# Kernel optimization log

Hardware: AMD Instinct MI355X
Metric: run time of the kernel (lower is better)

## Reference

```python
import jax, jax.numpy as jnp
import numpy as np

P, M, N, D, H, DFF = 20000, 20000, 16, 128, 8, 512
DPH = D // H
EPS = 1e-6
LN_EPS = 1e-5


def vn_linear(x, w):
    # x: (..., C_in, 3), w: (C_in, C_out) -> (..., C_out, 3)
    return jnp.einsum('...ci,co->...oi', x, w)


def vn_layernorm(x, gamma, beta):
    # x: (P, D, 3); layernorm over channel dim on vector norms, rescale directions
    n = jnp.linalg.norm(x, axis=-1)                      # (P, D)
    mu = jnp.mean(n, axis=-1, keepdims=True)
    var = jnp.var(n, axis=-1, keepdims=True)
    n_hat = (n - mu) / jnp.sqrt(var + LN_EPS) * gamma + beta
    return x * (n_hat / (n + EPS))[..., None]


def vn_relu(q, k):
    # VN nonlinearity: q, k: (..., C, 3); project q off negative half-space of k
    dot = jnp.sum(q * k, axis=-1, keepdims=True)         # (..., C, 1)
    ksq = jnp.sum(k * k, axis=-1, keepdims=True)
    return jnp.where(dot >= 0, q, q - (dot / (ksq + EPS)) * k)


def setup_inputs():
    key = jax.random.key(0)
    ks = jax.random.split(key, 24)
    s = lambda i, shp, scale: (jax.random.normal(ks[i], shp, jnp.float32) * scale)
    inp = {
        'tgt': s(0, (P, D * 3), 1.0),
        'memory': s(1, (M, D * 3), 1.0),
        'sh': s(2, (P, N + 1, 3), 1.0),
        'dist_atten': s(3, (P, N, H), 1.0),
        'Wq': s(4, (D, D), D ** -0.5),
        'Wk': s(5, (D, D), D ** -0.5),
        'Wv': s(6, (D, D), D ** -0.5),
        'Wo': s(7, (D, D), D ** -0.5),
        'g_w1': s(8, (D, H), D ** -0.5),
        'g_b1': jnp.zeros((H,), jnp.float32),
        'g_w2': s(9, (H, H), H ** -0.5),
        'g_b2': jnp.zeros((H,), jnp.float32),
        'ln1_g': jnp.ones((D,), jnp.float32),
        'ln1_b': jnp.zeros((D,), jnp.float32),
        'ln2_g': jnp.ones((D,), jnp.float32),
        'ln2_b': jnp.zeros((D,), jnp.float32),
        'ff_w1': s(10, (D, DFF), D ** -0.5),
        'ff_d1': s(11, (D, DFF), D ** -0.5),
        'ff_w2': s(12, (DFF, D), DFF ** -0.5),
        'index_pair': jax.random.randint(ks[13], (P, N), 0, M),
        'cnt1': jax.random.randint(ks[14], (P,), 0, N),
        'cnt2': jax.random.randint(ks[15], (P,), 0, N),
    }
    return inp


def reference(tgt, memory, sh, dist_atten, Wq, Wk, Wv, Wo,
              g_w1, g_b1, g_w2, g_b2, ln1_g, ln1_b, ln2_g, ln2_b,
              ff_w1, ff_d1, ff_w2, index_pair, cnt1, cnt2):
    x = tgt.reshape(P, D, 3)
    mem = memory.reshape(M, D, 3)
    q = vn_linear(x, Wq)                                  # (P, D, 3)
    k_all = vn_linear(mem, Wk)                            # (M, D, 3)
    v_all = vn_linear(mem, Wv)
    # irregular neighbor gather (ca_attention_mapper_v3)
    k = k_all[index_pair]                                 # (P, N, D, 3)
    v = v_all[index_pair]                                 # (P, N, D, 3)
    sh_n = sh[:, 1:].reshape(P, N, 1, 3)                  # drop l=0 term
    # multi-head dot attention on 3D vector features
    dot_atten = jnp.einsum('phdi,pnhdi->pnh',
                           q.reshape(P, H, DPH, 3),
                           k.reshape(P, N, H, DPH, 3))
    # spherical-harmonic position bias
    pos = jnp.sum((k - q[:, None]) * sh_n, axis=-1)       # (P, N, D)
    pos = jax.nn.relu(pos @ g_w1 + g_b1) @ g_w2 + g_b2    # (P, N, H)
    atten = (dot_atten + pos + dist_atten) / (DPH ** 0.5)
    atten = jax.nn.softmax(atten, axis=1)                 # softmax over neighbors
    tgt2 = jnp.einsum('pnh,pnhci->phci', atten,
                      v.reshape(P, N, H, DPH, 3)).reshape(P, D, 3)
    tgt2 = vn_linear(tgt2, Wo)
    y = vn_layernorm(x + tgt2, ln1_g, ln1_b)
    h1 = vn_relu(vn_linear(y, ff_w1), vn_linear(y, ff_d1))
    ff_out = vn_linear(h1, ff_w2)
    y = vn_layernorm(y + ff_out, ln2_g, ln2_b)
    return y.reshape(P, D * 3)
```

## Files before the change

### kernel.cpp

```cpp
#include <hip/hip_runtime.h>

#define PP 20000

typedef short short8 __attribute__((ext_vector_type(8)));
typedef float floatx4 __attribute__((ext_vector_type(4)));

__device__ __forceinline__ unsigned int bf16_rne_bits(float x){
    unsigned int xb = __float_as_uint(x);
    return (xb + 0x7FFFu + ((xb >> 16) & 1u)) & 0xFFFF0000u;
}
__device__ __forceinline__ void split2(float x, short &h, short &l){
    unsigned int hb = bf16_rne_bits(x);
    h = (short)(hb >> 16);
    float r = x - __uint_as_float(hb);
    l = (short)(bf16_rne_bits(r) >> 16);
}

__device__ __align__(16) short g_ff1[32*8192];
__device__ __align__(16) short g_ff2[16*8192];
__device__ __align__(16) short g_qkvo[4][4*8192];
__device__ __align__(16) float g_vvf[PP*128*4];

__global__ __launch_bounds__(256) void prep_weights(
    const float* __restrict__ Wq, const float* __restrict__ Wk,
    const float* __restrict__ Wv, const float* __restrict__ Wo,
    const float* __restrict__ W1, const float* __restrict__ Wd,
    const float* __restrict__ W2)
{
    const int tid = blockIdx.x*256 + threadIdx.x;
    for (int e = tid; e < 65536; e += 16384){
        int j = e & 7, kg = (e>>3) & 15, n = (e>>7) & 15, ch = e >> 11;
        int k = kg*8 + j, col = ch*16 + n;
        int pos = n*128 + ((kg ^ (n&7)) << 3) + j;
        short h, l;
        split2(W1[(size_t)k*512 + col], h, l);
        g_ff1[ch*8192 + pos]        = h;
        g_ff1[ch*8192 + 2048 + pos] = l;
        split2(Wd[(size_t)k*512 + col], h, l);
        g_ff1[ch*8192 + 4096 + pos] = h;
        g_ff1[ch*8192 + 6144 + pos] = l;
    }
    for (int e = tid; e < 65536; e += 16384){
        int w = e & 31, n2 = (e>>5) & 127, pair = e >> 12;
        int lslot = (w>>3) ^ ((n2>>1)&3);
        int k = pair*32 + lslot*8 + (w&7);
        short h, l; split2(W2[(size_t)k*128 + n2], h, l);
        g_ff2[pair*8192 + n2*32 + w]        = h;
        g_ff2[pair*8192 + 4096 + n2*32 + w] = l;
    }
    for (int e = tid; e < 65536; e += 16384){
        int w = e & 127, col = (e>>7) & 31, ch = (e>>12) & 3, wg = e >> 14;
        int lslot = (w>>3) ^ (col&7);
        int k = lslot*8 + (w&7);
        const float* Wsrc = (wg==0)?Wq:(wg==1)?Wk:(wg==2)?Wv:Wo;
        short h, l; split2(Wsrc[(size_t)k*128 + ch*32 + col], h, l);
        g_qkvo[wg][ch*8192 + col*128 + w]        = h;
        g_qkvo[wg][ch*8192 + 4096 + col*128 + w] = l;
    }
}

template<int VOUT>
__global__ __launch_bounds__(256) void vn_gemm_mfma_t(const float* __restrict__ in,
    int widx, float* __restrict__ out)
{
    __shared__ __align__(16) char pool[32768];
    short* Ysh = (short*)pool;
    short* Ysl = (short*)(pool + 16384);
    short* Bh  = (short*)pool;
    short* Bl  = (short*)(pool + 8192);

    const int tid  = threadIdx.x;
    const int wv   = tid >> 6;
    const int lane = tid & 63;
    const int mrow = lane & 15;
    const int kgrp = lane >> 4;
    const int p0   = blockIdx.x * 16;

    for (int f = tid; f < 2048; f += 256){
        int row = (f >> 7)*4 + 3, k = f & 127;
        Ysh[row*128 + k] = 0; Ysl[row*128 + k] = 0;
    }
    #pragma unroll
    for (int t = 0; t < 6; ++t){
        int f = tid + t*256;
        float4 w4 = *(const float4*)(in + (size_t)p0*384 + f*4);
        int e = f*4, pl = e/384, rem = e - pl*384;
        float vv4[4] = {w4.x, w4.y, w4.z, w4.w};
        #pragma unroll
        for (int j=0;j<4;++j){
            int c = (rem+j)/3, i = (rem+j) - c*3;
            int row = pl*4 + i;
            int idx = row*128 + (((c>>3) ^ (row&7)) << 3) + (c&7);
            short h, l; split2(vv4[j], h, l);
            Ysh[idx] = h; Ysl[idx] = l;
        }
    }
    __syncthreads();
    short8 ahf[4], alf[4];
    {
        const int arow = wv*16 + mrow;
        #pragma unroll
        for (int ks=0;ks<4;++ks){
            int slot = ks*4 + kgrp;
            int aoff = arow*128 + ((slot ^ (arow&7)) << 3);
            ahf[ks] = *(const short8*)(Ysh + aoff);
            alf[ks] = *(const short8*)(Ysl + aoff);
        }
    }

    const short* gW = g_qkvo[widx];
    for (int ch = 0; ch < 4; ++ch){
        __syncthreads();
        #pragma unroll
        for (int t=0;t<4;++t)
            ((short8*)pool)[tid + t*256] =
                ((const short8*)(gW + ch*8192))[tid + t*256];
        __syncthreads();

        #pragma unroll
        for (int ntl=0; ntl<2; ++ntl){
            floatx4 acc = {0.f,0.f,0.f,0.f};
            const int lcol = ntl*16 + mrow;
            #pragma unroll
            for (int ks=0;ks<4;++ks){
                int slot = ks*4 + kgrp;
                int boff = lcol*128 + ((slot ^ (mrow&7)) << 3);
                short8 bh = *(const short8*)(Bh + boff);
                short8 bl = *(const short8*)(Bl + boff);
                acc = __builtin_amdgcn_mfma_f32_16x16x32_bf16(ahf[ks], bh, acc, 0,0,0);
                acc = __builtin_amdgcn_mfma_f32_16x16x32_bf16(ahf[ks], bl, acc, 0,0,0);
                acc = __builtin_amdgcn_mfma_f32_16x16x32_bf16(alf[ks], bh, acc, 0,0,0);
            }
            const int p = p0 + wv*4 + kgrp;
            const int o = ch*32 + ntl*16 + mrow;
            if (VOUT == 0){
                size_t base = (size_t)p*384 + (size_t)o*3;
                out[base    ] = acc[0];
                out[base + 1] = acc[1];
                out[base + 2] = acc[2];
            } else {
                float4 v4;
                v4.x = acc[0]; v4.y = acc[1]; v4.z = acc[2]; v4.w = 0.f;
                *(float4*)(g_vvf + ((size_t)p*128 + o)*4) = v4;
            }
        }
    }
}

__global__ __launch_bounds__(256) void vn_gemm_ln_mfma(const float* __restrict__ in,
    const float* __restrict__ resid, const float* __restrict__ gamma,
    const float* __restrict__ beta, float* __restrict__ out)
{
    __shared__ __align__(16) char pool[32768];
    short* Ysh = (short*)pool;
    short* Ysl = (short*)(pool + 16384);
    short* Bh  = (short*)pool;
    short* Bl  = (short*)(pool + 8192);

    const int tid  = threadIdx.x;
    const int wv   = tid >> 6;
    const int lane = tid & 63;
    const int mrow = lane & 15;
    const int kgrp = lane >> 4;
    const int p0   = blockIdx.x * 16;

    for (int f = tid; f < 2048; f += 256){
        int row = (f >> 7)*4 + 3, k = f & 127;
        Ysh[row*128 + k] = 0; Ysl[row*128 + k] = 0;
    }
    #pragma unroll
    for (int t = 0; t < 6; ++t){
        int f = tid + t*256;
        float4 w4 = *(const float4*)(in + (size_t)p0*384 + f*4);
        int e = f*4, pl = e/384, rem = e - pl*384;
        float vv4[4] = {w4.x, w4.y, w4.z, w4.w};
        #pragma unroll
        for (int j=0;j<4;++j){
            int c = (rem+j)/3, i = (rem+j) - c*3;
            int row = pl*4 + i;
            int idx = row*128 + (((c>>3) ^ (row&7)) << 3) + (c&7);
            short h, l; split2(vv4[j], h, l);
            Ysh[idx] = h; Ysl[idx] = l;
        }
    }
    __syncthreads();
    short8 ahf[4], alf[4];
    {
        const int arow = wv*16 + mrow;
        #pragma unroll
        for (int ks=0;ks<4;++ks){
            int slot = ks*4 + kgrp;
            int aoff = arow*128 + ((slot ^ (arow&7)) << 3);
            ahf[ks] = *(const short8*)(Ysh + aoff);
            alf[ks] = *(const short8*)(Ysl + aoff);
        }
    }

    const int p = p0 + wv*4 + kgrp;
    float rx[8], ry[8], rz[8];
    const short* gW = g_qkvo[3];
    #pragma unroll
    for (int ch = 0; ch < 4; ++ch){
        __syncthreads();
        #pragma unroll
        for (int t=0;t<4;++t)
            ((short8*)pool)[tid + t*256] =
                ((const short8*)(gW + ch*8192))[tid + t*256];
        __syncthreads();

        #pragma unroll
        for (int ntl=0; ntl<2; ++ntl){
            floatx4 acc = {0.f,0.f,0.f,0.f};
            const int lcol = ntl*16 + mrow;
            #pragma unroll
            for (int ks=0;ks<4;++ks){
                int slot = ks*4 + kgrp;
                int boff = lcol*128 + ((slot ^ (mrow&7)) << 3);
                short8 bh = *(const short8*)(Bh + boff);
                short8 bl = *(const short8*)(Bl + boff);
                acc = __builtin_amdgcn_mfma_f32_16x16x32_bf16(ahf[ks], bh, acc, 0,0,0);
                acc = __builtin_amdgcn_mfma_f32_16x16x32_bf16(ahf[ks], bl, acc, 0,0,0);
                acc = __builtin_amdgcn_mfma_f32_16x16x32_bf16(alf[ks], bh, acc, 0,0,0);
            }
            const int s = ch*2 + ntl;
            const int o = ch*32 + ntl*16 + mrow;
            size_t base = (size_t)p*384 + (size_t)o*3;
            rx[s] = resid[base]   + acc[0];
            ry[s] = resid[base+1] + acc[1];
            rz[s] = resid[base+2] + acc[2];
        }
    }

    float nrm[8], s1 = 0.f, s2 = 0.f;
    #pragma unroll
    for (int s=0;s<8;++s){
        float n = sqrtf(rx[s]*rx[s] + ry[s]*ry[s] + rz[s]*rz[s]);
        nrm[s] = n; s1 += n; s2 += n*n;
    }
    #pragma unroll
    for (int m=1; m<16; m<<=1){
        s1 += __shfl_xor(s1, m);
        s2 += __shfl_xor(s2, m);
    }
    float mu  = s1*(1.f/128.f);
    float var = s2*(1.f/128.f) - mu*mu;
    float inv = rsqrtf(var + 1e-5f);
    #pragma unroll
    for (int s=0;s<8;++s){
        int o = (s>>1)*32 + (s&1)*16 + mrow;
        size_t base = (size_t)p*384 + (size_t)o*3;
        float nh = (nrm[s] - mu)*inv*gamma[o] + beta[o];
        float sc = nh/(nrm[s] + 1e-6f);
        out[base] = rx[s]*sc; out[base+1] = ry[s]*sc; out[base+2] = rz[s]*sc;
    }
}

__global__ __launch_bounds__(128) void attn_fused(
    float* io, const float* __restrict__ kf,
    const float* __restrict__ sh, const float* __restrict__ dist, const int* __restrict__ idxp,
    const float* __restrict__ gw1, const float* __restrict__ gb1,
    const float* __restrict__ gw2, const float* __restrict__ gb2)
{
    const int p = blockIdx.x, c = threadIdx.x;
    __shared__ __align__(16) float dot_s[16*132];
    __shared__ __align__(16) float pos_s[16*132];
    __shared__ float sh_s[48];
    __shared__ int   nidx[16];
    __shared__ __align__(16) float w1t[8*132];
    __shared__ float w2_s[64], b1_s[8], b2_s[8];
    __shared__ float u2_s[16*8], logit_s[16*8];
    __shared__ float att_s[128];

    if (c < 16) nidx[c] = idxp[p*16 + c];
    if (c < 48) sh_s[c] = sh[(size_t)p*51 + 3 + c];
    #pragma unroll
    for (int f = c; f < 1024; f += 128){
        int th2 = f >> 7, cc2 = f & 127;
        w1t[th2*132 + cc2] = gw1[cc2*8 + th2];
    }
    if (c < 64) w2_s[c] = gw2[c];
    if (c < 8){ b1_s[c]=gb1[c]; b2_s[c]=gb2[c]; }
    size_t qa = (size_t)p*384 + c*3;
    float qx = io[qa], qy = io[qa+1], qz = io[qa+2];
    __syncthreads();

    for (int n=0;n<16;++n){
        size_t kbase = (size_t)nidx[n]*384 + c*3;
        float kx = kf[kbase], ky = kf[kbase+1], kz = kf[kbase+2];
        dot_s[n*132 + c] = kx*qx + ky*qy + kz*qz;
        pos_s[n*132 + c] = (kx-qx)*sh_s[n*3] + (ky-qy)*sh_s[n*3+1] + (kz-qz)*sh_s[n*3+2];
    }
    __syncthreads();

    const int tn = c >> 3, th = c & 7;
    const float* drow = dot_s + tn*132 + th*16;
    float4 d0 = *(const float4*)(drow);
    float4 d1 = *(const float4*)(drow + 4);
    float4 d2 = *(const float4*)(drow + 8);
    float4 d3 = *(const float4*)(drow + 12);
    float dsum = (d0.x+d0.y+d0.z+d0.w) + (d1.x+d1.y+d1.z+d1.w)
               + (d2.x+d2.y+d2.z+d2.w) + (d3.x+d3.y+d3.z+d3.w);

    float uj = b1_s[th];
    const float* prow = pos_s + tn*132;
    const float* wrow = w1t  + th*132;
    #pragma unroll 8
    for (int cc=0; cc<128; cc+=4){
        float4 pv = *(const float4*)(prow + cc);
        float4 wv = *(const float4*)(wrow + cc);
        uj = fmaf(pv.x, wv.x, uj);
        uj = fmaf(pv.y, wv.y, uj);
        uj = fmaf(pv.z, wv.z, uj);
        uj = fmaf(pv.w, wv.w, uj);
    }
    u2_s[tn*8+th] = fmaxf(uj, 0.f);
    __syncthreads();

    float l = b2_s[th];
    #pragma unroll
    for (int j=0;j<8;++j) l += u2_s[tn*8+j]*w2_s[j*8+th];
    l += dsum + dist[(size_t)p*128 + tn*8 + th];
    logit_s[tn*8+th] = l * 0.25f;
    __syncthreads();

    if (c < 8){
        float mx = -3.0e38f;
        #pragma unroll
        for (int n=0;n<16;++n) mx = fmaxf(mx, logit_s[n*8+c]);
        float e[16], ssum = 0.f;
        #pragma unroll
        for (int n=0;n<16;++n){ e[n] = __expf(logit_s[n*8+c]-mx); ssum += e[n]; }
        float inv = 1.f/ssum;
        #pragma unroll
        for (int n=0;n<16;++n) att_s[n*8+c] = e[n]*inv;
    }
    __syncthreads();

    const int h = c >> 4;
    float ax=0.f, ay=0.f, az=0.f;
    #pragma unroll
    for (int n=0;n<16;++n){
        float wgt = att_s[n*8+h];
        float4 v4 = *(const float4*)(g_vvf + ((size_t)nidx[n]*128 + c)*4);
        ax += wgt*v4.x;
        ay += wgt*v4.y;
        az += wgt*v4.z;
    }
    size_t ob = (size_t)p*384 + c*3;
    io[ob] = ax; io[ob+1] = ay; io[ob+2] = az;
}

__global__ __launch_bounds__(256,2) void vn_ff_mfma(const float* __restrict__ in,
    const float* __restrict__ l2g, const float* __restrict__ l2b,
    float* __restrict__ out)
{
    __shared__ __align__(16) char pool[40960];
    short* Ws1h = (short*)(pool);
    short* Ws1l = (short*)(pool + 4096);
    short* Wsdh = (short*)(pool + 8192);
    short* Wsdl = (short*)(pool + 12288);
    short* Ws2h = (short*)(pool + 16384);
    short* Ws2l = (short*)(pool + 24576);
    short* Hsh  = (short*)(pool + 32768);
    short* Hsl  = (short*)(pool + 36864);
    short* Ysh  = (short*)(pool);
    short* Ysl  = (short*)(pool + 16384);

    const int tid  = threadIdx.x;
    const int wv   = tid >> 6;
    const int lane = tid & 63;
    const int mrow = lane & 15;
    const int kgrp = lane >> 4;
    const int p0   = blockIdx.x * 16;

    for (int f = tid; f < 2048; f += 256){
        int row = (f >> 7)*4 + 3, k = f & 127;
        Ysh[row*128 + k] = 0; Ysl[row*128 + k] = 0;
    }
    #pragma unroll
    for (int t = 0; t < 6; ++t){
        int f = tid + t*256;
        float4 w4 = *(const float4*)(in + (size_t)p0*384 + f*4);
        int e = f*4, pl = e/384, rem = e - pl*384;
        float vv4[4] = {w4.x, w4.y, w4.z, w4.w};
        #pragma unroll
        for (int j=0;j<4;++j){
            int c = (rem+j)/3, i = (rem+j) - c*3;
            int row = pl*4 + i;
            int idx = row*128 + (((c>>3) ^ (row&7)) << 3) + (c&7);
            short h, l; split2(vv4[j], h, l);
            Ysh[idx] = h; Ysl[idx] = l;
        }
    }
    __syncthreads();
    short8 ahf[4], alf[4];
    {
        const int arow = wv*16 + mrow;
        #pragma unroll
        for (int ks=0;ks<4;++ks){
            int slot = ks*4 + kgrp;
            int aoff = arow*128 + ((slot ^ (arow&7)) << 3);
            ahf[ks] = *(const short8*)(Ysh + aoff);
            alf[ks] = *(const short8*)(Ysl + aoff);
        }
    }

    floatx4 acc2[8];
    #pragma unroll
    for (int nt=0;nt<8;++nt) acc2[nt] = (floatx4){0.f,0.f,0.f,0.f};

    for (int ch = 0; ch < 32; ++ch){
        __syncthreads();
        #pragma unroll
        for (int t=0;t<4;++t)
            ((short8*)pool)[tid + t*256] =
                ((const short8*)(g_ff1 + ch*8192))[tid + t*256];
        if ((ch & 1) == 0){
            #pragma unroll
            for (int t=0;t<4;++t)
                ((short8*)(pool + 16384))[tid + t*256] =
                    ((const short8*)(g_ff2 + (ch>>1)*8192))[tid + t*256];
        }
        __syncthreads();

        floatx4 aU = {0.f,0.f,0.f,0.f}, aD = {0.f,0.f,0.f,0.f};
        #pragma unroll
        for (int ks=0;ks<4;++ks){
            int slot = ks*4 + kgrp;
            int boff = mrow*128 + ((slot ^ (mrow&7)) << 3);
            short8 b1h = *(const short8*)(Ws1h + boff);
            short8 b1l = *(const short8*)(Ws1l + boff);
            short8 bdh = *(const short8*)(Wsdh + boff);
            short8 bdl = *(const short8*)(Wsdl + boff);
            aU = __builtin_amdgcn_mfma_f32_16x16x32_bf16(ahf[ks], b1h, aU, 0,0,0);
            aU = __builtin_amdgcn_mfma_f32_16x16x32_bf16(ahf[ks], b1l, aU, 0,0,0);
            aU = __builtin_amdgcn_mfma_f32_16x16x32_bf16(alf[ks], b1h, aU, 0,0,0);
            aD = __builtin_amdgcn_mfma_f32_16x16x32_bf16(ahf[ks], bdh, aD, 0,0,0);
            aD = __builtin_amdgcn_mfma_f32_16x16x32_bf16(ahf[ks], bdl, aD, 0,0,0);
            aD = __builtin_amdgcn_mfma_f32_16x16x32_bf16(alf[ks], bdh, aD, 0,0,0);
        }

        {
            float ux=aU[0], uy=aU[1], uz=aU[2];
            float dx=aD[0], dy=aD[1], dz=aD[2];
            float dot = ux*dx + uy*dy + uz*dz;
            float ksq = dx*dx + dy*dy + dz*dz;
            if (dot < 0.f){
                float fc = dot/(ksq + 1e-6f);
                ux -= fc*dx; uy -= fc*dy; uz -= fc*dz;
            }
            int col  = (ch & 1)*16 + mrow;
            int slot = col >> 3, cl = col & 7;
            float hv[4] = {ux, uy, uz, 0.f};
            #pragma unroll
            for (int r=0;r<4;++r){
                int row = wv*16 + kgrp*4 + r;
                int idx = row*32 + ((slot ^ ((row>>1)&3)) << 3) + cl;
                short h, l; split2(hv[r], h, l);
                Hsh[idx] = h; Hsl[idx] = l;
            }
        }

        if (ch & 1){
            const int arow2 = wv*16 + mrow;
            int aoff = arow2*32 + ((kgrp ^ ((arow2>>1)&3)) << 3);
            short8 ah = *(const short8*)(Hsh + aoff);
            short8 al = *(const short8*)(Hsl + aoff);
            #pragma unroll
            for (int nt=0;nt<8;++nt){
                int bcol = nt*16 + mrow;
                int boff = bcol*32 + ((kgrp ^ ((bcol>>1)&3)) << 3);
                short8 bh = *(const short8*)(Ws2h + boff);
                short8 bl = *(const short8*)(Ws2l + boff);
                acc2[nt] = __builtin_amdgcn_mfma_f32_16x16x32_bf16(ah, bh, acc2[nt], 0,0,0);
                acc2[nt] = __builtin_amdgcn_mfma_f32_16x16x32_bf16(ah, bl, acc2[nt], 0,0,0);
                acc2[nt] = __builtin_amdgcn_mfma_f32_16x16x32_bf16(al, bh, acc2[nt], 0,0,0);
            }
        }
    }

    const int p = p0 + wv*4 + kgrp;
    float nrm[8];
    float s1 = 0.f, s2 = 0.f;
    #pragma unroll
    for (int nt=0;nt<8;++nt){
        int o = nt*16 + mrow;
        size_t base = (size_t)p*384 + (size_t)o*3;
        float rx = in[base]   + acc2[nt][0];
        float ry = in[base+1] + acc2[nt][1];
        float rz = in[base+2] + acc2[nt][2];
        float n = sqrtf(rx*rx + ry*ry + rz*rz);
        nrm[nt] = n;
        s1 += n; s2 += n*n;
    }
    #pragma unroll
    for (int m=1; m<16; m<<=1){
        s1 += __shfl_xor(s1, m);
        s2 += __shfl_xor(s2, m);
    }
    float mu  = s1*(1.f/128.f);
    float var = s2*(1.f/128.f) - mu*mu;
    float inv = rsqrtf(var + 1e-5f);
    #pragma unroll
    for (int nt=0;nt<8;++nt){
        int o = nt*16 + mrow;
        size_t base = (size_t)p*384 + (size_t)o*3;
        float rx = in[base]   + acc2[nt][0];
        float ry = in[base+1] + acc2[nt][1];
        float rz = in[base+2] + acc2[nt][2];
        float nh = (nrm[nt] - mu)*inv*l2g[o] + l2b[o];
        float sc = nh/(nrm[nt] + 1e-6f);
        out[base] = rx*sc; out[base+1] = ry*sc; out[base+2] = rz*sc;
    }
}

extern "C" void kernel_launch(void* const* d_in, const int* in_sizes, int n_in,
                              void* d_out, int out_size, void* d_ws, size_t ws_size,
                              hipStream_t stream)
{
    const float* tgt  = (const float*)d_in[0];
    const float* mem  = (const float*)d_in[1];
    const float* sh   = (const float*)d_in[2];
    const float* dist = (const float*)d_in[3];
    const float* Wq   = (const float*)d_in[4];
    const float* Wk   = (const float*)d_in[5];
    const float* Wv   = (const float*)d_in[6];
    const float* Wo   = (const float*)d_in[7];
    const float* gw1  = (const float*)d_in[8];
    const float* gb1  = (const float*)d_in[9];
    const float* gw2  = (const float*)d_in[10];
    const float* gb2  = (const float*)d_in[11];
    const float* ln1g = (const float*)d_in[12];
    const float* ln1b = (const float*)d_in[13];
    const float* ln2g = (const float*)d_in[14];
    const float* ln2b = (const float*)d_in[15];
    const float* fw1  = (const float*)d_in[16];
    const float* fd1  = (const float*)d_in[17];
    const float* fw2  = (const float*)d_in[18];
    const int*   idx  = (const int*)d_in[19];

    float* wsf = (float*)d_ws;
    float* outf = (float*)d_out;

    prep_weights<<<64,256,0,stream>>>(Wq, Wk, Wv, Wo, fw1, fd1, fw2);

    vn_gemm_mfma_t<0><<<1250,256,0,stream>>>(mem, 1, wsf);
    vn_gemm_mfma_t<1><<<1250,256,0,stream>>>(mem, 2, nullptr);
    vn_gemm_mfma_t<0><<<1250,256,0,stream>>>(tgt, 0, outf);
    attn_fused<<<PP,128,0,stream>>>(outf, wsf, sh, dist, idx, gw1, gb1, gw2, gb2);
    vn_gemm_ln_mfma<<<1250,256,0,stream>>>(outf, tgt, ln1g, ln1b, wsf);
    vn_ff_mfma<<<1250,256,0,stream>>>(wsf, ln2g, ln2b, outf);
}
```

Before: 505.7 us.

## Pack V buffer as 3-float vectors and reduce head dot products via shuffles

The V projection buffer changes from float4-padded (4 floats per channel) to a tight 3-float layout, cutting the gathered V bytes per neighbor by a quarter at the cost of scalar instead of 128-bit loads. Separately, the per-head dot-product sum now uses wavefront xor-shuffles over 16 lanes in registers instead of writing all 16x128 dot values to shared memory and re-reading them. This shrinks shared-memory footprint and traffic but adds 64 shuffles per thread.

```diff
diff --git a/kernel.cpp b/kernel.cpp
--- a/kernel.cpp
+++ b/kernel.cpp
@@ -19,7 +19,7 @@
 __device__ __align__(16) short g_ff1[32*8192];
 __device__ __align__(16) short g_ff2[16*8192];
 __device__ __align__(16) short g_qkvo[4][4*8192];
-__device__ __align__(16) float g_vvf[PP*128*4];
+__device__ __align__(16) float g_vvf[PP*384];
 
 __global__ __launch_bounds__(256) void prep_weights(
     const float* __restrict__ Wq, const float* __restrict__ Wk,
@@ -133,16 +133,11 @@
             }
             const int p = p0 + wv*4 + kgrp;
             const int o = ch*32 + ntl*16 + mrow;
-            if (VOUT == 0){
-                size_t base = (size_t)p*384 + (size_t)o*3;
-                out[base    ] = acc[0];
-                out[base + 1] = acc[1];
-                out[base + 2] = acc[2];
-            } else {
-                float4 v4;
-                v4.x = acc[0]; v4.y = acc[1]; v4.z = acc[2]; v4.w = 0.f;
-                *(float4*)(g_vvf + ((size_t)p*128 + o)*4) = v4;
-            }
+            size_t base = (size_t)p*384 + (size_t)o*3;
+            float* dst = (VOUT == 0) ? out : g_vvf;
+            dst[base    ] = acc[0];
+            dst[base + 1] = acc[1];
+            dst[base + 2] = acc[2];
         }
     }
 }
@@ -262,13 +257,13 @@
     const float* __restrict__ gw2, const float* __restrict__ gb2)
 {
     const int p = blockIdx.x, c = threadIdx.x;
-    __shared__ __align__(16) float dot_s[16*132];
     __shared__ __align__(16) float pos_s[16*132];
     __shared__ float sh_s[48];
     __shared__ int   nidx[16];
     __shared__ __align__(16) float w1t[8*132];
     __shared__ float w2_s[64], b1_s[8], b2_s[8];
     __shared__ float u2_s[16*8], logit_s[16*8];
+    __shared__ float dsum_s[16*8];
     __shared__ float att_s[128];
 
     if (c < 16) nidx[c] = idxp[p*16 + c];
@@ -284,23 +279,26 @@
     float qx = io[qa], qy = io[qa+1], qz = io[qa+2];
     __syncthreads();
 
+    float dreg[16];
+    #pragma unroll
     for (int n=0;n<16;++n){
         size_t kbase = (size_t)nidx[n]*384 + c*3;
         float kx = kf[kbase], ky = kf[kbase+1], kz = kf[kbase+2];
-        dot_s[n*132 + c] = kx*qx + ky*qy + kz*qz;
+        dreg[n] = kx*qx + ky*qy + kz*qz;
         pos_s[n*132 + c] = (kx-qx)*sh_s[n*3] + (ky-qy)*sh_s[n*3+1] + (kz-qz)*sh_s[n*3+2];
     }
+    #pragma unroll
+    for (int n=0;n<16;++n){
+        float v = dreg[n];
+        v += __shfl_xor(v, 1);
+        v += __shfl_xor(v, 2);
+        v += __shfl_xor(v, 4);
+        v += __shfl_xor(v, 8);
+        if ((c & 15) == n) dsum_s[n*8 + (c>>4)] = v;
+    }
     __syncthreads();
 
     const int tn = c >> 3, th = c & 7;
-    const float* drow = dot_s + tn*132 + th*16;
-    float4 d0 = *(const float4*)(drow);
-    float4 d1 = *(const float4*)(drow + 4);
-    float4 d2 = *(const float4*)(drow + 8);
-    float4 d3 = *(const float4*)(drow + 12);
-    float dsum = (d0.x+d0.y+d0.z+d0.w) + (d1.x+d1.y+d1.z+d1.w)
-               + (d2.x+d2.y+d2.z+d2.w) + (d3.x+d3.y+d3.z+d3.w);
-
     float uj = b1_s[th];
     const float* prow = pos_s + tn*132;
     const float* wrow = w1t  + th*132;
@@ -319,7 +317,7 @@
     float l = b2_s[th];
     #pragma unroll
     for (int j=0;j<8;++j) l += u2_s[tn*8+j]*w2_s[j*8+th];
-    l += dsum + dist[(size_t)p*128 + tn*8 + th];
+    l += dsum_s[tn*8+th] + dist[(size_t)p*128 + tn*8 + th];
     logit_s[tn*8+th] = l * 0.25f;
     __syncthreads();
 
@@ -341,10 +339,10 @@
     #pragma unroll
     for (int n=0;n<16;++n){
         float wgt = att_s[n*8+h];
-        float4 v4 = *(const float4*)(g_vvf + ((size_t)nidx[n]*128 + c)*4);
-        ax += wgt*v4.x;
-        ay += wgt*v4.y;
-        az += wgt*v4.z;
+        size_t vb = (size_t)nidx[n]*384 + c*3;
+        ax += wgt*g_vvf[vb];
+        ay += wgt*g_vvf[vb+1];
+        az += wgt*g_vvf[vb+2];
     }
     size_t ob = (size_t)p*384 + c*3;
     io[ob] = ax; io[ob+1] = ay; io[ob+2] = az;
```

New measurement: 478.7 us. -5.3%, faster.
